# Kernel tuning notes

Measured on AMD Instinct MI355X. Metric: run time of the kernel, lower is better.

## Reference

```python
import jax, jax.numpy as jnp
import numpy as np
import math

B, S, D, H = 8, 1024, 1024, 16
DK = D // H
DFF = 4 * D
EPS = 1e-5


def gelu_tanh(x):
    # matches the hand-written GELU: 0.5*x*(1+tanh(sqrt(2/pi)*(x+0.044715*x^3)))
    c = math.sqrt(2.0 / math.pi)
    return 0.5 * x * (1.0 + jnp.tanh(c * (x + 0.044715 * x ** 3)))


def layernorm(x, g, b):
    # faithful to the custom LayerNorm: unbiased std (ddof=1), eps added to std
    mean = jnp.mean(x, -1, keepdims=True)
    std = jnp.std(x, -1, keepdims=True, ddof=1)
    return g * (x - mean) / (std + EPS) + b


def setup_inputs() -> dict:
    key = jax.random.key(0)
    ks = jax.random.split(key, 12)
    sc_d = 1.0 / math.sqrt(D)
    sc_f = 1.0 / math.sqrt(DFF)
    inp = {
        "x": jax.random.normal(ks[0], (B, S, D), jnp.float32),
        "mask": jax.random.randint(ks[1], (B, 1, S, S), 0, 2, jnp.int32),
        "wq": jax.random.normal(ks[2], (D, D), jnp.float32) * sc_d,
        "bq": jnp.zeros((D,), jnp.float32),
        "wk": jax.random.normal(ks[3], (D, D), jnp.float32) * sc_d,
        "bk": jnp.zeros((D,), jnp.float32),
        "wv": jax.random.normal(ks[4], (D, D), jnp.float32) * sc_d,
        "bv": jnp.zeros((D,), jnp.float32),
        "wo": jax.random.normal(ks[5], (D, D), jnp.float32) * sc_d,
        "bo": jnp.zeros((D,), jnp.float32),
        "w1": jax.random.normal(ks[6], (DFF, D), jnp.float32) * sc_d,
        "b1": jnp.zeros((DFF,), jnp.float32),
        "w2": jax.random.normal(ks[7], (D, DFF), jnp.float32) * sc_f,
        "b2": jnp.zeros((D,), jnp.float32),
        "ln1_g": jnp.ones((D,), jnp.float32),
        "ln1_b": jnp.zeros((D,), jnp.float32),
        "ln2_g": jnp.ones((D,), jnp.float32),
        "ln2_b": jnp.zeros((D,), jnp.float32),
    }
    return inp


def _mha(xn, mask, wq, bq, wk, bk, wv, bv, wo, bo):
    def proj(w, b):
        y = xn @ w.T + b                       # [B,S,D]
        return y.reshape(B, S, H, DK).transpose(0, 2, 1, 3)  # [B,H,S,DK]
    q, k, v = proj(wq, bq), proj(wk, bk), proj(wv, bv)
    scores = jnp.einsum("bhqd,bhkd->bhqk", q, k) / math.sqrt(DK)
    scores = jnp.where(mask == 0, -1e9, scores)
    p = jax.nn.softmax(scores, axis=-1)
    o = jnp.einsum("bhqk,bhkd->bhqd", p, v)    # [B,H,S,DK]
    o = o.transpose(0, 2, 1, 3).reshape(B, S, D)
    return o @ wo.T + bo


def reference(x, mask, wq, bq, wk, bk, wv, bv, wo, bo, w1, b1, w2, b2,
              ln1_g, ln1_b, ln2_g, ln2_b):
    # dropout is identity in eval mode
    xn = layernorm(x, ln1_g, ln1_b)
    x = x + _mha(xn, mask, wq, bq, wk, bk, wv, bv, wo, bo)
    xn = layernorm(x, ln2_g, ln2_b)
    ff = gelu_tanh(xn @ w1.T + b1) @ w2.T + b2
    return x + ff
```

## Files before the change

### kernel.cpp

```cpp
#include <hip/hip_runtime.h>
#include <stdint.h>

typedef float f32x4 __attribute__((ext_vector_type(4)));
typedef short short8 __attribute__((ext_vector_type(8)));
typedef __bf16 bf16x8 __attribute__((ext_vector_type(8)));

static __device__ __forceinline__ short f2bf(float f) {
  unsigned u = __builtin_bit_cast(unsigned, f);
  u = (u + 0x7FFFu + ((u >> 16) & 1u)) >> 16;
  return (short)u;
}

static __device__ __forceinline__ unsigned pack2bf(float a, float b) {
  return ((unsigned)(unsigned short)f2bf(a)) |
         (((unsigned)(unsigned short)f2bf(b)) << 16);
}

static __device__ __forceinline__ f32x4 mfma16(short8 a, short8 b, f32x4 c) {
  return __builtin_amdgcn_mfma_f32_16x16x32_bf16(
      __builtin_bit_cast(bf16x8, a), __builtin_bit_cast(bf16x8, b), c, 0, 0, 0);
}

static __device__ __forceinline__ void gld_lds16(const void* g, void* s) {
  __builtin_amdgcn_global_load_lds(
      (const __attribute__((address_space(1))) void*)g,
      (__attribute__((address_space(3))) void*)s, 16, 0, 0);
}

__global__ __launch_bounds__(256) void cvt_f2bf(const float* __restrict__ in,
                                                short* __restrict__ out, int n4) {
  int i = blockIdx.x * 256 + threadIdx.x;
  if (i < n4) {
    float4 v = ((const float4*)in)[i];
    short4 o;
    o.x = f2bf(v.x); o.y = f2bf(v.y); o.z = f2bf(v.z); o.w = f2bf(v.w);
    ((short4*)out)[i] = o;
  }
}

__global__ __launch_bounds__(256) void packmask(const int* __restrict__ m,
                                                unsigned* __restrict__ out) {
  int w = blockIdx.x * 256 + threadIdx.x;
  const int4* p = (const int4*)(m + (size_t)w * 32);
  unsigned bits = 0;
#pragma unroll
  for (int c = 0; c < 8; c++) {
    int4 v = p[c];
    bits |= (unsigned)(v.x != 0) << (c * 4 + 0);
    bits |= (unsigned)(v.y != 0) << (c * 4 + 1);
    bits |= (unsigned)(v.z != 0) << (c * 4 + 2);
    bits |= (unsigned)(v.w != 0) << (c * 4 + 3);
  }
  out[w] = bits;
}

__global__ __launch_bounds__(256) void ln_bf16(const float* __restrict__ x,
                                               const float* __restrict__ g,
                                               const float* __restrict__ bb,
                                               short* __restrict__ out) {
  const int row = blockIdx.x, tid = threadIdx.x;
  const float4 xv = *(const float4*)&x[(size_t)row * 1024 + tid * 4];
  float s = xv.x + xv.y + xv.z + xv.w;
#pragma unroll
  for (int o = 32; o; o >>= 1) s += __shfl_down(s, o);
  __shared__ float red[8];
  if ((tid & 63) == 0) red[tid >> 6] = s;
  __syncthreads();
  const float mean = (red[0] + red[1] + red[2] + red[3]) * (1.f / 1024.f);
  const float a0 = xv.x - mean, a1 = xv.y - mean, a2 = xv.z - mean, a3 = xv.w - mean;
  float ss = a0 * a0 + a1 * a1 + a2 * a2 + a3 * a3;
#pragma unroll
  for (int o = 32; o; o >>= 1) ss += __shfl_down(ss, o);
  if ((tid & 63) == 0) red[4 + (tid >> 6)] = ss;
  __syncthreads();
  const float inv =
      1.f / (sqrtf((red[4] + red[5] + red[6] + red[7]) * (1.f / 1023.f)) + 1e-5f);
  const float4 gv = *(const float4*)&g[tid * 4];
  const float4 bv = *(const float4*)&bb[tid * 4];
  short4 o4;
  o4.x = f2bf(gv.x * a0 * inv + bv.x);
  o4.y = f2bf(gv.y * a1 * inv + bv.y);
  o4.z = f2bf(gv.z * a2 * inv + bv.z);
  o4.w = f2bf(gv.w * a3 * inv + bv.w);
  *(short4*)&out[(size_t)row * 1024 + tid * 4] = o4;
}

template <int ACT, int RES, int OBF>
__global__ __launch_bounds__(256) void gemm_bt(
    const short* __restrict__ A, const short* __restrict__ Bw,
    const float* __restrict__ bias, const float* __restrict__ resid,
    void* __restrict__ Cout, int M, int N, int K) {
  __shared__ alignas(1024) short As[128 * 32];
  __shared__ alignas(1024) short Bs[128 * 32];
  const int tid = threadIdx.x;
  const int l = tid & 63, w = tid >> 6;
  const int wr = w >> 1, wc = w & 1;
  const int m0 = blockIdx.y * 128, n0 = blockIdx.x * 128;
  const int fr = l & 15, fq = l >> 4;
  const size_t Ksz = (size_t)K;

  const short* ag = A + (size_t)(m0 + w * 32 + (l >> 2)) * Ksz + (l & 3) * 8;
  const short* bg = Bw + (size_t)(n0 + w * 32 + (l >> 2)) * Ksz + (l & 3) * 8;
  short* asw = As + w * 1024;
  short* bsw = Bs + w * 1024;

  f32x4 acc[4][4] = {};

  for (int kt = 0; kt < K; kt += 32) {
    gld_lds16(ag + kt, asw);
    gld_lds16(ag + kt + 16 * Ksz, asw + 512);
    gld_lds16(bg + kt, bsw);
    gld_lds16(bg + kt + 16 * Ksz, bsw + 512);
    __syncthreads();
    short8 af[4], bf[4];
#pragma unroll
    for (int m = 0; m < 4; m++)
      af[m] = *(const short8*)&As[(wr * 64 + m * 16 + fr) * 32 + fq * 8];
#pragma unroll
    for (int n = 0; n < 4; n++)
      bf[n] = *(const short8*)&Bs[(wc * 64 + n * 16 + fr) * 32 + fq * 8];
#pragma unroll
    for (int m = 0; m < 4; m++)
#pragma unroll
      for (int n = 0; n < 4; n++) acc[m][n] = mfma16(af[m], bf[n], acc[m][n]);
    __syncthreads();
  }

#pragma unroll
  for (int m = 0; m < 4; m++) {
#pragma unroll
    for (int n = 0; n < 4; n++) {
      const int row = m0 + wr * 64 + m * 16 + fq * 4;
      const int col = n0 + wc * 64 + n * 16 + fr;
      const float bvl = bias[col];
#pragma unroll
      for (int r = 0; r < 4; r++) {
        float v = acc[m][n][r] + bvl;
        if (ACT == 1) {
          float zz = 0.7978845608028654f * (v + 0.044715f * v * v * v);
          float th = 1.f - 2.f / (__expf(2.f * zz) + 1.f);
          v = 0.5f * v * (1.f + th);
        }
        if (RES) v += resid[(size_t)(row + r) * N + col];
        if (OBF)
          ((short*)Cout)[(size_t)(row + r) * N + col] = f2bf(v);
        else
          ((float*)Cout)[(size_t)(row + r) * N + col] = v;
      }
    }
  }
}

__global__ __launch_bounds__(256, 4) void attn_fwd(
    const short* __restrict__ Qm, const short* __restrict__ Km,
    const short* __restrict__ Vm, const unsigned* __restrict__ MW,
    short* __restrict__ Om) {
  const int orig = blockIdx.x;
  const int gid = (orig & 7) * 256 + (orig >> 3);
  const int qt = gid & 15;
  const int h = (gid >> 4) & 15;
  const int b = gid >> 8;
  const int tid = threadIdx.x, l = tid & 63, w = tid >> 6;
  const int fr = l & 15, fq = l >> 4;
  __shared__ alignas(1024) short Ks[2][64 * 64];
  __shared__ alignas(1024) short Vt[2][64 * 64];
  __shared__ alignas(1024) short Ps[4][16 * 64];
  const int qbase = qt * 64;

  short8 qf0, qf1;
  {
    const short* qp = Qm + ((size_t)b * 1024 + qbase + w * 16 + fr) * 1024 + h * 64 + fq * 8;
    qf0 = *(const short8*)qp;
    qf1 = *(const short8*)(qp + 32);
  }
  f32x4 m2 = {-1e30f, -1e30f, -1e30f, -1e30f};
  f32x4 lsum = {};
  f32x4 oacc[4] = {};

  const int kcol = (l & 7) ^ ((l >> 3) & 7);
  const short* kg =
      Km + ((size_t)b * 1024 + w * 16 + (l >> 3)) * 1024 + h * 64 + kcol * 8;
  const int vkey = w * 16 + (l >> 2), vd0 = (l & 3) * 16;
  const short* vg = Vm + ((size_t)b * 1024 + vkey) * 1024 + h * 64 + vd0;
  const int keyp = ((vkey >= 32) ? 32 : 0) + (l >> 2) * 2 + (w & 1);
  const int kslot = keyp >> 3, kbyte = keyp & 7;
  const unsigned* mwp = MW + ((size_t)b * 1024 + qbase + w * 16 + fq * 4) * 32;

  gld_lds16(kg, &Ks[0][w * 1024]);
  gld_lds16(kg + 8 * 1024, &Ks[0][w * 1024 + 512]);
  short8 vv0 = *(const short8*)vg;
  short8 vv1 = *(const short8*)(vg + 8);
#pragma unroll
  for (int e = 0; e < 8; e++)
    Vt[0][(vd0 + e) * 64 + ((kslot ^ (e & 7)) << 3) + kbyte] = vv0[e];
#pragma unroll
  for (int e = 0; e < 8; e++)
    Vt[0][(vd0 + 8 + e) * 64 + ((kslot ^ (e & 7)) << 3) + kbyte] = vv1[e];
  __syncthreads();

  for (int t = 0; t < 16; t++) {
    const int cur = t & 1;
    if (t < 15) {
      const short* kgn = kg + (size_t)(t + 1) * 64 * 1024;
      gld_lds16(kgn, &Ks[cur ^ 1][w * 1024]);
      gld_lds16(kgn + 8 * 1024, &Ks[cur ^ 1][w * 1024 + 512]);
      const short* vgn = vg + (size_t)(t + 1) * 64 * 1024;
      vv0 = *(const short8*)vgn;
      vv1 = *(const short8*)(vgn + 8);
    }
    f32x4 sv[4];
    __builtin_amdgcn_s_setprio(1);
#pragma unroll
    for (int j = 0; j < 4; j++) {
      const int row = j * 16 + fr;
      short8 k0 = *(const short8*)&Ks[cur][row * 64 + ((fq ^ (fr & 7)) << 3)];
      short8 k1 = *(const short8*)&Ks[cur][row * 64 + (((4 + fq) ^ (fr & 7)) << 3)];
      f32x4 z = {0.f, 0.f, 0.f, 0.f};
      sv[j] = mfma16(qf0, k0, z);
      sv[j] = mfma16(qf1, k1, sv[j]);
    }
    __builtin_amdgcn_s_setprio(0);
#pragma unroll
    for (int r = 0; r < 4; r++) {
      const uint2 mw = *(const uint2*)(mwp + (size_t)r * 32 + t * 2);
      float t0 = ((mw.x >> fr) & 1u) ? sv[0][r] * 0.125f : -3e38f;
      float t1 = ((mw.x >> (16 + fr)) & 1u) ? sv[1][r] * 0.125f : -3e38f;
      float t2 = ((mw.y >> fr) & 1u) ? sv[2][r] * 0.125f : -3e38f;
      float t3 = ((mw.y >> (16 + fr)) & 1u) ? sv[3][r] * 0.125f : -3e38f;
      const float pmax = fmaxf(fmaxf(t0, t1), fmaxf(t2, t3));
      if (!__all(pmax <= m2[r] + 8.f)) {
        float mx = pmax;
        mx = fmaxf(mx, __shfl_xor(mx, 1));
        mx = fmaxf(mx, __shfl_xor(mx, 2));
        mx = fmaxf(mx, __shfl_xor(mx, 4));
        mx = fmaxf(mx, __shfl_xor(mx, 8));
        const float nm = fmaxf(m2[r], mx);
        const float al = __expf(m2[r] - nm);
        m2[r] = nm;
        lsum[r] *= al;
#pragma unroll
        for (int dt = 0; dt < 4; dt++) oacc[dt][r] *= al;
      }
      const float p0 = __expf(t0 - m2[r]);
      const float p1 = __expf(t1 - m2[r]);
      const float p2 = __expf(t2 - m2[r]);
      const float p3 = __expf(t3 - m2[r]);
      float ts = (p0 + p1) + (p2 + p3);
      ts += __shfl_xor(ts, 1);
      ts += __shfl_xor(ts, 2);
      ts += __shfl_xor(ts, 4);
      ts += __shfl_xor(ts, 8);
      lsum[r] += ts;
      const int q = fq * 4 + r;
      const int s0 = (fr >> 2) ^ (q & 7);
      const int s1 = (4 + (fr >> 2)) ^ (q & 7);
      *(unsigned*)&Ps[w][q * 64 + (s0 << 3) + ((fr & 3) << 1)] = pack2bf(p0, p1);
      *(unsigned*)&Ps[w][q * 64 + (s1 << 3) + ((fr & 3) << 1)] = pack2bf(p2, p3);
    }
    short8 pa0 = *(const short8*)&Ps[w][fr * 64 + ((fq ^ (fr & 7)) << 3)];
    short8 pa1 = *(const short8*)&Ps[w][fr * 64 + (((4 + fq) ^ (fr & 7)) << 3)];
    __builtin_amdgcn_s_setprio(1);
#pragma unroll
    for (int dt = 0; dt < 4; dt++) {
      const int row = dt * 16 + fr;
      short8 v0 = *(const short8*)&Vt[cur][row * 64 + ((fq ^ (fr & 7)) << 3)];
      short8 v1 = *(const short8*)&Vt[cur][row * 64 + (((4 + fq) ^ (fr & 7)) << 3)];
      oacc[dt] = mfma16(pa0, v0, oacc[dt]);
      oacc[dt] = mfma16(pa1, v1, oacc[dt]);
    }
    __builtin_amdgcn_s_setprio(0);
    if (t < 15) {
#pragma unroll
      for (int e = 0; e < 8; e++)
        Vt[cur ^ 1][(vd0 + e) * 64 + ((kslot ^ (e & 7)) << 3) + kbyte] = vv0[e];
#pragma unroll
      for (int e = 0; e < 8; e++)
        Vt[cur ^ 1][(vd0 + 8 + e) * 64 + ((kslot ^ (e & 7)) << 3) + kbyte] = vv1[e];
    }
    __syncthreads();
  }

#pragma unroll
  for (int dt = 0; dt < 4; dt++) {
#pragma unroll
    for (int r = 0; r < 4; r++) {
      const size_t qrow = (size_t)b * 1024 + qbase + w * 16 + fq * 4 + r;
      Om[qrow * 1024 + h * 64 + dt * 16 + fr] = f2bf(oacc[dt][r] / lsum[r]);
    }
  }
}

extern "C" void kernel_launch(void* const* d_in, const int* in_sizes, int n_in,
                              void* d_out, int out_size, void* d_ws, size_t ws_size,
                              hipStream_t stream) {
  (void)in_sizes; (void)n_in; (void)out_size; (void)ws_size;
  const float* x   = (const float*)d_in[0];
  const int*   msk = (const int*)d_in[1];
  const float* wq  = (const float*)d_in[2];
  const float* bq  = (const float*)d_in[3];
  const float* wk  = (const float*)d_in[4];
  const float* bk  = (const float*)d_in[5];
  const float* wv  = (const float*)d_in[6];
  const float* bv  = (const float*)d_in[7];
  const float* wo  = (const float*)d_in[8];
  const float* bo  = (const float*)d_in[9];
  const float* w1  = (const float*)d_in[10];
  const float* b1  = (const float*)d_in[11];
  const float* w2  = (const float*)d_in[12];
  const float* b2  = (const float*)d_in[13];
  const float* g1  = (const float*)d_in[14];
  const float* be1 = (const float*)d_in[15];
  const float* g2  = (const float*)d_in[16];
  const float* be2 = (const float*)d_in[17];
  float* out = (float*)d_out;

  char* p = (char*)d_ws;
  auto take = [&](size_t n) { char* r = p; p += (n + 1023) & ~(size_t)1023; return r; };
  const size_t MD = (size_t)8192 * 1024;
  short* XN = (short*)take(MD * 2);
  short* Qb = (short*)take(MD * 2);
  short* Kb = (short*)take(MD * 2);
  short* Vb = (short*)take(MD * 2);
  float* X1 = (float*)take(MD * 4);
  short* F1 = (short*)take((size_t)8192 * 4096 * 2);
  unsigned* MW = (unsigned*)take((size_t)8 * 1024 * 32 * 4);
  short* WQ = (short*)take((size_t)1024 * 1024 * 2);
  short* WK = (short*)take((size_t)1024 * 1024 * 2);
  short* WV = (short*)take((size_t)1024 * 1024 * 2);
  short* WO = (short*)take((size_t)1024 * 1024 * 2);
  short* W1 = (short*)take((size_t)4096 * 1024 * 2);
  short* W2 = (short*)take((size_t)1024 * 4096 * 2);

  cvt_f2bf<<<1024, 256, 0, stream>>>(wq, WQ, 262144);
  cvt_f2bf<<<1024, 256, 0, stream>>>(wk, WK, 262144);
  cvt_f2bf<<<1024, 256, 0, stream>>>(wv, WV, 262144);
  cvt_f2bf<<<1024, 256, 0, stream>>>(wo, WO, 262144);
  cvt_f2bf<<<4096, 256, 0, stream>>>(w1, W1, 1048576);
  cvt_f2bf<<<4096, 256, 0, stream>>>(w2, W2, 1048576);
  packmask<<<1024, 256, 0, stream>>>(msk, MW);
  ln_bf16<<<8192, 256, 0, stream>>>(x, g1, be1, XN);
  gemm_bt<0, 0, 1><<<dim3(8, 64), 256, 0, stream>>>(XN, WQ, bq, nullptr, Qb, 8192, 1024, 1024);
  gemm_bt<0, 0, 1><<<dim3(8, 64), 256, 0, stream>>>(XN, WK, bk, nullptr, Kb, 8192, 1024, 1024);
  gemm_bt<0, 0, 1><<<dim3(8, 64), 256, 0, stream>>>(XN, WV, bv, nullptr, Vb, 8192, 1024, 1024);
  attn_fwd<<<2048, 256, 0, stream>>>(Qb, Kb, Vb, MW, Qb);
  gemm_bt<0, 1, 0><<<dim3(8, 64), 256, 0, stream>>>(Qb, WO, bo, x, X1, 8192, 1024, 1024);
  ln_bf16<<<8192, 256, 0, stream>>>(X1, g2, be2, XN);
  gemm_bt<1, 0, 1><<<dim3(32, 64), 256, 0, stream>>>(XN, W1, b1, nullptr, F1, 8192, 4096, 1024);
  gemm_bt<0, 1, 0><<<dim3(8, 64), 256, 0, stream>>>(F1, W2, b2, X1, out, 8192, 1024, 4096);
}
```

Before: 664.8 us.

## Fuse QKV projections into one GEMM and trim attention softmax overhead

Concatenates the Q, K and V weights and biases so a single 8192x3072 GEMM writes an interleaved QKV buffer, and attention reads it with a 3072 row stride. Inside attention, the 1/sqrt(dk) scale is folded into Q before the QK product. The per-tile row-sum shuffles are deferred to one reduction after the loop. An extra XOR swizzle is added to the transposed V layout in LDS to reduce bank conflicts. These cut kernel launches, per-tile shuffle and multiply work, and LDS conflicts, at the cost of rounding the scaled Q to bf16 once more and reusing one large workspace buffer for both QKV and F1.

```diff
diff --git a/kernel.cpp b/kernel.cpp
--- a/kernel.cpp
+++ b/kernel.cpp
@@ -9,6 +9,10 @@
   unsigned u = __builtin_bit_cast(unsigned, f);
   u = (u + 0x7FFFu + ((u >> 16) & 1u)) >> 16;
   return (short)u;
+}
+
+static __device__ __forceinline__ float bf2f(short s) {
+  return __builtin_bit_cast(float, (unsigned)((unsigned short)s) << 16);
 }
 
 static __device__ __forceinline__ unsigned pack2bf(float a, float b) {
@@ -36,6 +40,15 @@
     o.x = f2bf(v.x); o.y = f2bf(v.y); o.z = f2bf(v.z); o.w = f2bf(v.w);
     ((short4*)out)[i] = o;
   }
+}
+
+__global__ __launch_bounds__(256) void concat3(const float* __restrict__ a,
+                                               const float* __restrict__ b,
+                                               const float* __restrict__ c,
+                                               float* __restrict__ o) {
+  int i = blockIdx.x * 256 + threadIdx.x;
+  float v = (i < 1024) ? a[i] : ((i < 2048) ? b[i - 1024] : c[i - 2048]);
+  o[i] = v;
 }
 
 __global__ __launch_bounds__(256) void packmask(const int* __restrict__ m,
@@ -152,8 +165,7 @@
 }
 
 __global__ __launch_bounds__(256, 4) void attn_fwd(
-    const short* __restrict__ Qm, const short* __restrict__ Km,
-    const short* __restrict__ Vm, const unsigned* __restrict__ MW,
+    const short* __restrict__ QKV, const unsigned* __restrict__ MW,
     short* __restrict__ Om) {
   const int orig = blockIdx.x;
   const int gid = (orig & 7) * 256 + (orig >> 3);
@@ -166,12 +178,19 @@
   __shared__ alignas(1024) short Vt[2][64 * 64];
   __shared__ alignas(1024) short Ps[4][16 * 64];
   const int qbase = qt * 64;
+  const size_t RS = 3072;
 
   short8 qf0, qf1;
   {
-    const short* qp = Qm + ((size_t)b * 1024 + qbase + w * 16 + fr) * 1024 + h * 64 + fq * 8;
+    const short* qp =
+        QKV + ((size_t)(b * 1024 + qbase + w * 16 + fr)) * RS + h * 64 + fq * 8;
     qf0 = *(const short8*)qp;
     qf1 = *(const short8*)(qp + 32);
+#pragma unroll
+    for (int e = 0; e < 8; e++) {
+      qf0[e] = f2bf(0.125f * bf2f(qf0[e]));
+      qf1[e] = f2bf(0.125f * bf2f(qf1[e]));
+    }
   }
   f32x4 m2 = {-1e30f, -1e30f, -1e30f, -1e30f};
   f32x4 lsum = {};
@@ -179,32 +198,33 @@
 
   const int kcol = (l & 7) ^ ((l >> 3) & 7);
   const short* kg =
-      Km + ((size_t)b * 1024 + w * 16 + (l >> 3)) * 1024 + h * 64 + kcol * 8;
+      QKV + ((size_t)(b * 1024 + w * 16 + (l >> 3))) * RS + 1024 + h * 64 + kcol * 8;
   const int vkey = w * 16 + (l >> 2), vd0 = (l & 3) * 16;
-  const short* vg = Vm + ((size_t)b * 1024 + vkey) * 1024 + h * 64 + vd0;
+  const short* vg = QKV + ((size_t)(b * 1024 + vkey)) * RS + 2048 + h * 64 + vd0;
   const int keyp = ((vkey >= 32) ? 32 : 0) + (l >> 2) * 2 + (w & 1);
   const int kslot = keyp >> 3, kbyte = keyp & 7;
-  const unsigned* mwp = MW + ((size_t)b * 1024 + qbase + w * 16 + fq * 4) * 32;
+  const int vxk = (l & 3) << 1;
+  const unsigned* mwp = MW + ((size_t)(b * 1024 + qbase + w * 16 + fq * 4)) * 32;
 
   gld_lds16(kg, &Ks[0][w * 1024]);
-  gld_lds16(kg + 8 * 1024, &Ks[0][w * 1024 + 512]);
+  gld_lds16(kg + 8 * RS, &Ks[0][w * 1024 + 512]);
   short8 vv0 = *(const short8*)vg;
   short8 vv1 = *(const short8*)(vg + 8);
 #pragma unroll
   for (int e = 0; e < 8; e++)
-    Vt[0][(vd0 + e) * 64 + ((kslot ^ (e & 7)) << 3) + kbyte] = vv0[e];
+    Vt[0][(vd0 + e) * 64 + ((kslot ^ (e & 7) ^ vxk) << 3) + kbyte] = vv0[e];
 #pragma unroll
   for (int e = 0; e < 8; e++)
-    Vt[0][(vd0 + 8 + e) * 64 + ((kslot ^ (e & 7)) << 3) + kbyte] = vv1[e];
+    Vt[0][(vd0 + 8 + e) * 64 + ((kslot ^ (e & 7) ^ vxk) << 3) + kbyte] = vv1[e];
   __syncthreads();
 
   for (int t = 0; t < 16; t++) {
     const int cur = t & 1;
     if (t < 15) {
-      const short* kgn = kg + (size_t)(t + 1) * 64 * 1024;
+      const short* kgn = kg + (size_t)(t + 1) * 64 * RS;
       gld_lds16(kgn, &Ks[cur ^ 1][w * 1024]);
-      gld_lds16(kgn + 8 * 1024, &Ks[cur ^ 1][w * 1024 + 512]);
-      const short* vgn = vg + (size_t)(t + 1) * 64 * 1024;
+      gld_lds16(kgn + 8 * RS, &Ks[cur ^ 1][w * 1024 + 512]);
+      const short* vgn = vg + (size_t)(t + 1) * 64 * RS;
       vv0 = *(const short8*)vgn;
       vv1 = *(const short8*)(vgn + 8);
     }
@@ -223,10 +243,10 @@
 #pragma unroll
     for (int r = 0; r < 4; r++) {
       const uint2 mw = *(const uint2*)(mwp + (size_t)r * 32 + t * 2);
-      float t0 = ((mw.x >> fr) & 1u) ? sv[0][r] * 0.125f : -3e38f;
-      float t1 = ((mw.x >> (16 + fr)) & 1u) ? sv[1][r] * 0.125f : -3e38f;
-      float t2 = ((mw.y >> fr) & 1u) ? sv[2][r] * 0.125f : -3e38f;
-      float t3 = ((mw.y >> (16 + fr)) & 1u) ? sv[3][r] * 0.125f : -3e38f;
+      float t0 = ((mw.x >> fr) & 1u) ? sv[0][r] : -3e38f;
+      float t1 = ((mw.x >> (16 + fr)) & 1u) ? sv[1][r] : -3e38f;
+      float t2 = ((mw.y >> fr) & 1u) ? sv[2][r] : -3e38f;
+      float t3 = ((mw.y >> (16 + fr)) & 1u) ? sv[3][r] : -3e38f;
       const float pmax = fmaxf(fmaxf(t0, t1), fmaxf(t2, t3));
       if (!__all(pmax <= m2[r] + 8.f)) {
         float mx = pmax;
@@ -245,12 +265,7 @@
       const float p1 = __expf(t1 - m2[r]);
       const float p2 = __expf(t2 - m2[r]);
       const float p3 = __expf(t3 - m2[r]);
-      float ts = (p0 + p1) + (p2 + p3);
-      ts += __shfl_xor(ts, 1);
-      ts += __shfl_xor(ts, 2);
-      ts += __shfl_xor(ts, 4);
-      ts += __shfl_xor(ts, 8);
-      lsum[r] += ts;
+      lsum[r] += (p0 + p1) + (p2 + p3);
       const int q = fq * 4 + r;
       const int s0 = (fr >> 2) ^ (q & 7);
       const int s1 = (4 + (fr >> 2)) ^ (q & 7);
@@ -263,8 +278,10 @@
 #pragma unroll
     for (int dt = 0; dt < 4; dt++) {
       const int row = dt * 16 + fr;
-      short8 v0 = *(const short8*)&Vt[cur][row * 64 + ((fq ^ (fr & 7)) << 3)];
-      short8 v1 = *(const short8*)&Vt[cur][row * 64 + (((4 + fq) ^ (fr & 7)) << 3)];
+      const int vkx = dt << 1;
+      short8 v0 = *(const short8*)&Vt[cur][row * 64 + ((fq ^ (fr & 7) ^ vkx) << 3)];
+      short8 v1 =
+          *(const short8*)&Vt[cur][row * 64 + (((4 + fq) ^ (fr & 7) ^ vkx) << 3)];
       oacc[dt] = mfma16(pa0, v0, oacc[dt]);
       oacc[dt] = mfma16(pa1, v1, oacc[dt]);
     }
@@ -272,12 +289,23 @@
     if (t < 15) {
 #pragma unroll
       for (int e = 0; e < 8; e++)
-        Vt[cur ^ 1][(vd0 + e) * 64 + ((kslot ^ (e & 7)) << 3) + kbyte] = vv0[e];
+        Vt[cur ^ 1][(vd0 + e) * 64 + ((kslot ^ (e & 7) ^ vxk) << 3) + kbyte] = vv0[e];
 #pragma unroll
       for (int e = 0; e < 8; e++)
-        Vt[cur ^ 1][(vd0 + 8 + e) * 64 + ((kslot ^ (e & 7)) << 3) + kbyte] = vv1[e];
+        Vt[cur ^ 1][(vd0 + 8 + e) * 64 + ((kslot ^ (e & 7) ^ vxk) << 3) + kbyte] =
+            vv1[e];
     }
     __syncthreads();
+  }
+
+#pragma unroll
+  for (int r = 0; r < 4; r++) {
+    float s = lsum[r];
+    s += __shfl_xor(s, 1);
+    s += __shfl_xor(s, 2);
+    s += __shfl_xor(s, 4);
+    s += __shfl_xor(s, 8);
+    lsum[r] = s;
   }
 
 #pragma unroll
@@ -317,34 +345,35 @@
   char* p = (char*)d_ws;
   auto take = [&](size_t n) { char* r = p; p += (n + 1023) & ~(size_t)1023; return r; };
   const size_t MD = (size_t)8192 * 1024;
-  short* XN = (short*)take(MD * 2);
-  short* Qb = (short*)take(MD * 2);
-  short* Kb = (short*)take(MD * 2);
-  short* Vb = (short*)take(MD * 2);
-  float* X1 = (float*)take(MD * 4);
-  short* F1 = (short*)take((size_t)8192 * 4096 * 2);
+  short* XN  = (short*)take(MD * 2);
+  short* BIG = (short*)take((size_t)8192 * 4096 * 2);
+  short* QKV = BIG;
+  short* F1  = BIG;
+  short* AO  = (short*)take(MD * 2);
+  float* X1  = (float*)take(MD * 4);
   unsigned* MW = (unsigned*)take((size_t)8 * 1024 * 32 * 4);
-  short* WQ = (short*)take((size_t)1024 * 1024 * 2);
-  short* WK = (short*)take((size_t)1024 * 1024 * 2);
-  short* WV = (short*)take((size_t)1024 * 1024 * 2);
-  short* WO = (short*)take((size_t)1024 * 1024 * 2);
-  short* W1 = (short*)take((size_t)4096 * 1024 * 2);
-  short* W2 = (short*)take((size_t)1024 * 4096 * 2);
-
-  cvt_f2bf<<<1024, 256, 0, stream>>>(wq, WQ, 262144);
-  cvt_f2bf<<<1024, 256, 0, stream>>>(wk, WK, 262144);
-  cvt_f2bf<<<1024, 256, 0, stream>>>(wv, WV, 262144);
+  short* WQKV = (short*)take((size_t)3072 * 1024 * 2);
+  short* WO  = (short*)take((size_t)1024 * 1024 * 2);
+  short* W1  = (short*)take((size_t)4096 * 1024 * 2);
+  short* W2  = (short*)take((size_t)1024 * 4096 * 2);
+  float* BQKV = (float*)take((size_t)3072 * 4);
+
+  cvt_f2bf<<<1024, 256, 0, stream>>>(wq, WQKV, 262144);
+  cvt_f2bf<<<1024, 256, 0, stream>>>(wk, WQKV + (size_t)1024 * 1024, 262144);
+  cvt_f2bf<<<1024, 256, 0, stream>>>(wv, WQKV + (size_t)2048 * 1024, 262144);
   cvt_f2bf<<<1024, 256, 0, stream>>>(wo, WO, 262144);
   cvt_f2bf<<<4096, 256, 0, stream>>>(w1, W1, 1048576);
   cvt_f2bf<<<4096, 256, 0, stream>>>(w2, W2, 1048576);
+  concat3<<<12, 256, 0, stream>>>(bq, bk, bv, BQKV);
   packmask<<<1024, 256, 0, stream>>>(msk, MW);
   ln_bf16<<<8192, 256, 0, stream>>>(x, g1, be1, XN);
-  gemm_bt<0, 0, 1><<<dim3(8, 64), 256, 0, stream>>>(XN, WQ, bq, nullptr, Qb, 8192, 1024, 1024);
-  gemm_bt<0, 0, 1><<<dim3(8, 64), 256, 0, stream>>>(XN, WK, bk, nullptr, Kb, 8192, 1024, 1024);
-  gemm_bt<0, 0, 1><<<dim3(8, 64), 256, 0, stream>>>(XN, WV, bv, nullptr, Vb, 8192, 1024, 1024);
-  attn_fwd<<<2048, 256, 0, stream>>>(Qb, Kb, Vb, MW, Qb);
-  gemm_bt<0, 1, 0><<<dim3(8, 64), 256, 0, stream>>>(Qb, WO, bo, x, X1, 8192, 1024, 1024);
+  gemm_bt<0, 0, 1><<<dim3(24, 64), 256, 0, stream>>>(XN, WQKV, BQKV, nullptr, QKV,
+                                                     8192, 3072, 1024);
+  attn_fwd<<<2048, 256, 0, stream>>>(QKV, MW, AO);
+  gemm_bt<0, 1, 0><<<dim3(8, 64), 256, 0, stream>>>(AO, WO, bo, x, X1, 8192, 1024, 1024);
   ln_bf16<<<8192, 256, 0, stream>>>(X1, g2, be2, XN);
-  gemm_bt<1, 0, 1><<<dim3(32, 64), 256, 0, stream>>>(XN, W1, b1, nullptr, F1, 8192, 4096, 1024);
-  gemm_bt<0, 1, 0><<<dim3(8, 64), 256, 0, stream>>>(F1, W2, b2, X1, out, 8192, 1024, 4096);
-}
+  gemm_bt<1, 0, 1><<<dim3(32, 64), 256, 0, stream>>>(XN, W1, b1, nullptr, F1,
+                                                     8192, 4096, 1024);
+  gemm_bt<0, 1, 0><<<dim3(8, 64), 256, 0, stream>>>(F1, W2, b2, X1, out,
+                                                    8192, 1024, 4096);
+}
```

New measurement: 615.3 us. 1.08x faster.
